# Performance work log

Measured on AMD Instinct MI355X. Metric: run time of the kernel, lower is better.

## Reference

```python
import jax, jax.numpy as jnp
import numpy as np

B, N, D, E, L = 8, 4096, 256, 65536, 1  # graphs, padded nodes, d_model, padded edges, num_layers


def setup_inputs() -> dict:
    key = jax.random.key(0)
    ks = jax.random.split(key, 9)
    x = jax.random.normal(ks[0], (B, N, D), dtype=jnp.float32)
    edge_index = jax.random.randint(ks[1], (B, 2, E), 0, N)
    edge_weight = jax.random.uniform(ks[2], (B, E), dtype=jnp.float32)
    mask = jax.random.randint(ks[3], (B, N), 0, 2).astype(jnp.int32)
    s = 1.0 / np.sqrt(D)
    # GatedGraphConv per-layer linear weight [L, D, D]
    W = jax.random.uniform(ks[4], (L, D, D), jnp.float32, -s, s)
    # GRUCell parameters (r, z, n stacked)
    W_ih = jax.random.uniform(ks[5], (3 * D, D), jnp.float32, -s, s)
    W_hh = jax.random.uniform(ks[6], (3 * D, D), jnp.float32, -s, s)
    b_ih = jax.random.uniform(ks[7], (3 * D,), jnp.float32, -s, s)
    b_hh = jax.random.uniform(ks[8], (3 * D,), jnp.float32, -s, s)
    return {"x": x, "edge_index": edge_index, "edge_weight": edge_weight,
            "mask": mask, "W": W, "W_ih": W_ih, "W_hh": W_hh,
            "b_ih": b_ih, "b_hh": b_hh}


def _gated_graph_conv(x, u, v, ew, W, W_ih, W_hh, b_ih, b_hh):
    """x:[B,N,D]; u,v:[B,E] src/dst indices; ew:[B,E] (already masked)."""
    h = x
    for l in range(L):
        m = jnp.einsum('bnd,de->bne', h, W[l])            # linear transform
        msg = jnp.take_along_axis(m, u[..., None], axis=1) * ew[..., None]  # [B,E,D]
        agg = jax.vmap(lambda ms, vi: jax.ops.segment_sum(ms, vi, num_segments=N))(msg, v)
        # GRUCell(input=agg, hidden=h)
        gi = agg @ W_ih.T + b_ih                          # [B,N,3D]
        gh = h @ W_hh.T + b_hh
        r = jax.nn.sigmoid(gi[..., :D] + gh[..., :D])
        z = jax.nn.sigmoid(gi[..., D:2 * D] + gh[..., D:2 * D])
        n = jnp.tanh(gi[..., 2 * D:] + r * gh[..., 2 * D:])
        h = (1.0 - z) * n + z * h
    return h


def reference(x, edge_index, edge_weight, mask, W, W_ih, W_hh, b_ih, b_hh):
    node_valid = mask > 0                                  # [B,N]
    u = edge_index[:, 0]                                   # source
    v = edge_index[:, 1]                                   # target
    # Drop edges touching invalid nodes: weight -> 0 (equivalent under sum aggr)
    e_valid = jnp.take_along_axis(node_valid, u, axis=1) & jnp.take_along_axis(node_valid, v, axis=1)
    ew = edge_weight * e_valid.astype(edge_weight.dtype)
    h = _gated_graph_conv(x, u, v, ew, W, W_ih, W_hh, b_ih, b_hh)
    # Invalid nodes stay zero (original writes only valid rows of a zeros output)
    return h * node_valid[..., None].astype(h.dtype)
```

## Files before the change

### kernel.cpp

```cpp
#include <hip/hip_runtime.h>
#include <math.h>

#define Bn 8
#define Nn 4096
#define Dn 256
#define En 65536
#define CAP 48

typedef __bf16 bf8 __attribute__((ext_vector_type(8)));
typedef float f4 __attribute__((ext_vector_type(4)));
typedef unsigned short us8 __attribute__((ext_vector_type(8)));

__device__ __forceinline__ float4 ld4(const float* p) { return *(const float4*)p; }

__device__ __forceinline__ unsigned short f2bf(float f) {
    union { float f; unsigned int u; } v; v.f = f;
    unsigned int r = v.u + 0x7fff + ((v.u >> 16) & 1);
    return (unsigned short)(r >> 16);
}
__device__ __forceinline__ float bf2f(unsigned short h) {
    union { unsigned int u; float f; } v; v.u = (unsigned int)h << 16;
    return v.f;
}


__device__ __forceinline__ void stage16c(const unsigned short* __restrict__ gchunk,
                                         int stride, char* ldschunk, int lane) {
    int u = lane >> 3, s = lane & 7;
    int xx = s ^ (u & 7);
    const unsigned short* g = gchunk + (size_t)(2 * u + (xx >> 2)) * stride + (xx & 3) * 8;
    __builtin_amdgcn_global_load_lds((const __attribute__((address_space(1))) void*)g,
                                     (__attribute__((address_space(3))) void*)ldschunk,
                                     16, 0, 0);
}

__device__ __forceinline__ bf8 fragld(const unsigned short* region, int r, int q) {
    int s = (((r & 1) << 2) | q) ^ ((r >> 1) & 7);
    return *(const bf8*)(region + (r >> 1) * 64 + s * 8);
}

__device__ __forceinline__ void ldswrite8(unsigned short* region, int r, int q,
                                          const unsigned short* vals) {
    int s = (((r & 1) << 2) | q) ^ ((r >> 1) & 7);
    *(us8*)(region + (r >> 1) * 64 + s * 8) = *(const us8*)vals;
}


__device__ void rowscan_piece(const int* __restrict__ mask, int* __restrict__ rowidx,
                              int* __restrict__ rowcnt, int* part) {
    int t = threadIdx.x;
    int base = t * 128;
    unsigned long long b0 = 0, b1 = 0;
    int s = 0;
#pragma unroll 8
    for (int i = 0; i < 64; i++) {
        int m = mask[base + i] > 0;
        b0 |= (unsigned long long)m << i; s += m;
    }
#pragma unroll 8
    for (int i = 0; i < 64; i++) {
        int m = mask[base + 64 + i] > 0;
        b1 |= (unsigned long long)m << i; s += m;
    }
    part[t] = s;
    __syncthreads();
    for (int st = 1; st < 256; st <<= 1) {
        int v = (t >= st) ? part[t - st] : 0;
        __syncthreads();
        part[t] += v;
        __syncthreads();
    }
    int run = part[t] - s;
    for (int i = 0; i < 64; i++)
        if ((b0 >> i) & 1) rowidx[run++] = base + i;
    for (int i = 0; i < 64; i++)
        if ((b1 >> i) & 1) rowidx[run++] = base + 64 + i;
    if (t == 255) rowcnt[0] = part[255];
}

__device__ void wf_piece(int wfi, const float* __restrict__ Wih, const float* __restrict__ W,
                         unsigned short* __restrict__ Ball, unsigned short* lds) {
    int t = threadIdx.x, lane = t & 63, w = t >> 6;
    int wr = w >> 1, wc = w & 1, q = lane >> 4, c16 = lane & 15;
    int o0 = (wfi % 6) * 128, d0b = (wfi / 6) * 64;
    f4 acc[4][2];
    f4 zz = {0.f, 0.f, 0.f, 0.f};
#pragma unroll
    for (int rt = 0; rt < 4; rt++)
#pragma unroll
        for (int ct = 0; ct < 2; ct++) acc[rt][ct] = zz;

    int r = t >> 1, half = t & 1;
    for (int k0 = 0; k0 < 256; k0 += 32) {
        const float* pa = Wih + (size_t)(o0 + r) * 256 + k0 + half * 16;
        float4 a0 = ld4(pa), a1 = ld4(pa + 4), a2 = ld4(pa + 8), a3 = ld4(pa + 12);
        float4 b0, b1, b2, b3;
        if (t < 128) {
            const float* pb = W + (size_t)(d0b + r) * 256 + k0 + half * 16;
            b0 = ld4(pb); b1 = ld4(pb + 4); b2 = ld4(pb + 8); b3 = ld4(pb + 12);
        }
        __syncthreads();
        unsigned short tmp[16];
        tmp[0] = f2bf(a0.x); tmp[1] = f2bf(a0.y); tmp[2] = f2bf(a0.z); tmp[3] = f2bf(a0.w);
        tmp[4] = f2bf(a1.x); tmp[5] = f2bf(a1.y); tmp[6] = f2bf(a1.z); tmp[7] = f2bf(a1.w);
        tmp[8] = f2bf(a2.x); tmp[9] = f2bf(a2.y); tmp[10] = f2bf(a2.z); tmp[11] = f2bf(a2.w);
        tmp[12] = f2bf(a3.x); tmp[13] = f2bf(a3.y); tmp[14] = f2bf(a3.z); tmp[15] = f2bf(a3.w);
        ldswrite8(lds, r, half * 2, tmp);
        ldswrite8(lds, r, half * 2 + 1, tmp + 8);
        if (t < 128) {
            unsigned short tb[16];
            tb[0] = f2bf(b0.x); tb[1] = f2bf(b0.y); tb[2] = f2bf(b0.z); tb[3] = f2bf(b0.w);
            tb[4] = f2bf(b1.x); tb[5] = f2bf(b1.y); tb[6] = f2bf(b1.z); tb[7] = f2bf(b1.w);
            tb[8] = f2bf(b2.x); tb[9] = f2bf(b2.y); tb[10] = f2bf(b2.z); tb[11] = f2bf(b2.w);
            tb[12] = f2bf(b3.x); tb[13] = f2bf(b3.y); tb[14] = f2bf(b3.z); tb[15] = f2bf(b3.w);
            ldswrite8(lds + 4096, r, half * 2, tb);
            ldswrite8(lds + 4096, r, half * 2 + 1, tb + 8);
        }
        __syncthreads();
        bf8 a[4];
#pragma unroll
        for (int rt = 0; rt < 4; rt++) a[rt] = fragld(lds, wr * 64 + rt * 16 + c16, q);
#pragma unroll
        for (int ct = 0; ct < 2; ct++) {
            bf8 b = fragld(lds + 4096, wc * 32 + ct * 16 + c16, q);
#pragma unroll
            for (int rt = 0; rt < 4; rt++)
                acc[rt][ct] = __builtin_amdgcn_mfma_f32_16x16x32_bf16(a[rt], b, acc[rt][ct], 0, 0, 0);
        }
    }
#pragma unroll
    for (int ct = 0; ct < 2; ct++) {
        int col = d0b + wc * 32 + ct * 16 + c16;
#pragma unroll
        for (int rt = 0; rt < 4; rt++) {
            int ob = o0 + wr * 64 + rt * 16 + q * 4;
#pragma unroll
            for (int i = 0; i < 4; i++)
                Ball[(size_t)(ob + i) * 512 + col] = f2bf(acc[rt][ct][i]);
        }
    }
}

__global__ __launch_bounds__(256) void setup_kernel(const int* __restrict__ ei,
                                                    const int* __restrict__ mask,
                                                    const float* __restrict__ Wih,
                                                    const float* __restrict__ W,
                                                    const float* __restrict__ Whh,
                                                    const float* __restrict__ ew,
                                                    int* __restrict__ cnt,
                                                    int2* __restrict__ bucket,
                                                    int* __restrict__ rowidx,
                                                    int* __restrict__ rowcnt,
                                                    unsigned short* __restrict__ Ball,
                                                    float* __restrict__ out) {
    __shared__ __align__(16) unsigned short lds[6144];
    int b = blockIdx.x, t = threadIdx.x;
    if (b == 0) {
        rowscan_piece(mask, rowidx, rowcnt, (int*)lds);
        return;
    }
    if (b < 25) {
        wf_piece(b - 1, Wih, W, Ball, lds);
        return;
    }
    if (b < 217) {
        int i = ((b - 25) * 256 + t) * 4;
        float4 wv = ld4(Whh + i);
        int o = i >> 8, d = i & 255;
        ushort4 ov;
        ov.x = f2bf(wv.x); ov.y = f2bf(wv.y); ov.z = f2bf(wv.z); ov.w = f2bf(wv.w);
        *(ushort4*)(Ball + (size_t)o * 512 + 256 + d) = ov;
        return;
    }
    if (b < 2265) {
        int idx = (b - 217) * 256 + t;
        int bb = idx >> 16, e = idx & 65535;
        const int* eb = ei + (size_t)bb * 2 * En;
        int u = eb[e];
        int v = eb[En + e];
        const int* mb = mask + bb * Nn;
        if (mb[u] > 0 && mb[v] > 0) {
            int pos = atomicAdd(&cnt[bb * Nn + v], 1);
            if (pos < CAP) {
                int2 pr;
                pr.x = u;
                pr.y = __float_as_int(ew[(size_t)bb * En + e]);
                bucket[(size_t)(bb * Nn + v) * CAP + pos] = pr;
            }
        }
        return;
    }
    {
        int zb = b - 2265;
        int r = zb * 8 + (t >> 5);
        if (mask[r] > 0) return;
        int col = (t & 31) * 8;
        float4 z = make_float4(0.f, 0.f, 0.f, 0.f);
        *(float4*)(out + (size_t)r * 256 + col) = z;
        *(float4*)(out + (size_t)r * 256 + col + 4) = z;
    }
}


__global__ __launch_bounds__(256) void agg_kernel(const float* __restrict__ x,
                                                  const int* __restrict__ cnt,
                                                  const int2* __restrict__ bucket,
                                                  const int* __restrict__ rowidx,
                                                  const int* __restrict__ rowcnt,
                                                  unsigned short* __restrict__ Ac) {
    int wave = threadIdx.x >> 6, lane = threadIdx.x & 63;
    int i = blockIdx.x * 4 + wave;
    if (i >= rowcnt[0]) return;
    int v = rowidx[i];
    int b = v >> 12, n = v & 4095;
    int m = cnt[b * Nn + n];
    m = m < CAP ? m : CAP;
    const int2* bk = bucket + (size_t)(b * Nn + n) * CAP;
    const float* Xb = x + (size_t)b * Nn * 256;
    float a0 = 0.f, a1 = 0.f, a2 = 0.f, a3 = 0.f;
    for (int j = 0; j < m; j += 8) {
        int u[8]; float wv[8];
#pragma unroll
        for (int k = 0; k < 8; k++) {
            int jj = j + k;
            bool ok = jj < m;
            int2 pr = bk[ok ? jj : 0];
            u[k] = pr.x;
            wv[k] = ok ? __int_as_float(pr.y) : 0.f;
        }
        float4 mv[8];
#pragma unroll
        for (int k = 0; k < 8; k++) mv[k] = ld4(Xb + (size_t)u[k] * 256 + lane * 4);
#pragma unroll
        for (int k = 0; k < 8; k++) {
            a0 += wv[k] * mv[k].x; a1 += wv[k] * mv[k].y;
            a2 += wv[k] * mv[k].z; a3 += wv[k] * mv[k].w;
        }
    }
    ushort4 o;
    o.x = f2bf(a0); o.y = f2bf(a1); o.z = f2bf(a2); o.w = f2bf(a3);
    *(ushort4*)(Ac + (size_t)i * 512 + lane * 4) = o;
    float4 xv = ld4(x + (size_t)v * 256 + lane * 4);
    ushort4 xo;
    xo.x = f2bf(xv.x); xo.y = f2bf(xv.y); xo.z = f2bf(xv.z); xo.w = f2bf(xv.w);
    *(ushort4*)(Ac + (size_t)i * 512 + 256 + lane * 4) = xo;
}


#define GRU_STAGE(kk, bufbase)                                                      \
    {                                                                               \
        if (w < 4) {                                                                \
            _Pragma("unroll") for (int j = 0; j < 3; j++) {                         \
                int c = w * 3 + j;                                                  \
                const unsigned short* src;                                          \
                if (c < 8)                                                          \
                    src = Ac + (size_t)(row0 + c * 16) * 512 + (kk) * 32;           \
                else {                                                              \
                    int g = (c - 8) >> 2, cg = (c - 8) & 3;                         \
                    src = Ball + (size_t)(g * 256 + d0 + cg * 16) * 512 + (kk) * 32;\
                }                                                                   \
                stage16c(src, 512, (char*)(bufbase) + c * 1024, lane);              \
            }                                                                       \
        } else {                                                                    \
            _Pragma("unroll") for (int j = 0; j < 2; j++) {                         \
                int c = 12 + (w - 4) * 2 + j;                                       \
                int g = (c - 8) >> 2, cg = (c - 8) & 3;                             \
                const unsigned short* src =                                         \
                    Ball + (size_t)(g * 256 + d0 + cg * 16) * 512 + (kk) * 32;      \
                stage16c(src, 512, (char*)(bufbase) + c * 1024, lane);              \
            }                                                                       \
        }                                                                           \
    }

#define GRU_COMPUTE(bufbase, ACCM)                                                  \
    {                                                                               \
        const unsigned short* rb = (bufbase);                                       \
        bf8 a0 = fragld(rb + (wr * 2) * 512, c16, q);                               \
        bf8 a1 = fragld(rb + (wr * 2 + 1) * 512, c16, q);                           \
        _Pragma("unroll") for (int ct = 0; ct < 2; ct++) {                          \
            int cg = wc * 2 + ct;                                                   \
            bf8 br = fragld(rb + (8 + cg) * 512, c16, q);                           \
            bf8 bz = fragld(rb + (12 + cg) * 512, c16, q);                          \
            bf8 bm = fragld(rb + (16 + cg) * 512, c16, q);                          \
            acc_r[0][ct] = __builtin_amdgcn_mfma_f32_16x16x32_bf16(a0, br, acc_r[0][ct], 0, 0, 0); \
            acc_r[1][ct] = __builtin_amdgcn_mfma_f32_16x16x32_bf16(a1, br, acc_r[1][ct], 0, 0, 0); \
            acc_z[0][ct] = __builtin_amdgcn_mfma_f32_16x16x32_bf16(a0, bz, acc_z[0][ct], 0, 0, 0); \
            acc_z[1][ct] = __builtin_amdgcn_mfma_f32_16x16x32_bf16(a1, bz, acc_z[1][ct], 0, 0, 0); \
            ACCM[0][ct] = __builtin_amdgcn_mfma_f32_16x16x32_bf16(a0, bm, ACCM[0][ct], 0, 0, 0);   \
            ACCM[1][ct] = __builtin_amdgcn_mfma_f32_16x16x32_bf16(a1, bm, ACCM[1][ct], 0, 0, 0);   \
        }                                                                           \
    }

#define GRU_WAITV(n04, n47)                                                         \
    if (w < 4) { asm volatile("s_waitcnt vmcnt(" #n04 ")" ::: "memory"); }          \
    else       { asm volatile("s_waitcnt vmcnt(" #n47 ")" ::: "memory"); }          \
    __builtin_amdgcn_sched_barrier(0);

#define GRU_STEP(kk, STAGEBUF, COMPBUF, ACCM, n04, n47)                             \
    __builtin_amdgcn_s_barrier();             \
    GRU_STAGE((kk) + 2, STAGEBUF)                                                   \
    GRU_WAITV(n04, n47)                             \
    __builtin_amdgcn_s_barrier();                   \
    __builtin_amdgcn_s_setprio(1);                                                  \
    GRU_COMPUTE(COMPBUF, ACCM)                                                      \
    __builtin_amdgcn_s_setprio(0);                                                  \
    __builtin_amdgcn_sched_barrier(0);

#define GRU_STEP_LAST(kk, COMPBUF, ACCM, n04, n47)                                  \
    __builtin_amdgcn_s_barrier();                                                   \
    GRU_WAITV(n04, n47)                                                             \
    __builtin_amdgcn_s_barrier();                                                   \
    __builtin_amdgcn_s_setprio(1);                                                  \
    GRU_COMPUTE(COMPBUF, ACCM)                                                      \
    __builtin_amdgcn_s_setprio(0);                                                  \
    __builtin_amdgcn_sched_barrier(0);

__global__ __launch_bounds__(512, 4) void gru_kernel(const unsigned short* __restrict__ Ac,
                                                     const unsigned short* __restrict__ Ball,
                                                     const float* __restrict__ bih,
                                                     const float* __restrict__ bhh,
                                                     const int* __restrict__ rowidx,
                                                     const int* __restrict__ rowcnt,
                                                     float* __restrict__ out) {
    __shared__ __align__(16) unsigned short lds[30720];
    const int t = threadIdx.x;
    const int lane = t & 63, w = t >> 6;
    const int wr = w >> 1, wc = w & 1;
    const int q = lane >> 4, c16 = lane & 15;
    const int row0 = blockIdx.x * 128, d0 = blockIdx.y * 64;
    const int cnt = rowcnt[0];
    if (row0 >= cnt) return;

    f4 acc_r[2][2], acc_z[2][2], acc_gn[2][2], acc_hn[2][2];
    f4 zz = {0.f, 0.f, 0.f, 0.f};
#pragma unroll
    for (int rt = 0; rt < 2; rt++)
#pragma unroll
        for (int ct = 0; ct < 2; ct++) {
            acc_r[rt][ct] = zz; acc_z[rt][ct] = zz;
            acc_gn[rt][ct] = zz; acc_hn[rt][ct] = zz;
        }

    unsigned short* bufA = lds;
    unsigned short* bufB = lds + 10240;
    unsigned short* bufC = lds + 20480;

    GRU_STAGE(0, bufA)
    GRU_STAGE(1, bufB)

    GRU_STEP(0,  bufC, bufA, acc_gn, 6, 4)
    GRU_STEP(1,  bufA, bufB, acc_gn, 6, 4)
    GRU_STEP(2,  bufB, bufC, acc_gn, 6, 4)
    GRU_STEP(3,  bufC, bufA, acc_gn, 6, 4)
    GRU_STEP(4,  bufA, bufB, acc_gn, 6, 4)
    GRU_STEP(5,  bufB, bufC, acc_gn, 6, 4)
    GRU_STEP(6,  bufC, bufA, acc_gn, 6, 4)
    GRU_STEP(7,  bufA, bufB, acc_gn, 6, 4)
    GRU_STEP(8,  bufB, bufC, acc_hn, 6, 4)
    GRU_STEP(9,  bufC, bufA, acc_hn, 6, 4)
    GRU_STEP(10, bufA, bufB, acc_hn, 6, 4)
    GRU_STEP(11, bufB, bufC, acc_hn, 6, 4)
    GRU_STEP(12, bufC, bufA, acc_hn, 6, 4)
    GRU_STEP(13, bufA, bufB, acc_hn, 6, 4)
    GRU_STEP_LAST(14, bufC, acc_hn, 3, 2)
    GRU_STEP_LAST(15, bufA, acc_hn, 0, 0)

#pragma unroll
    for (int ct = 0; ct < 2; ct++) {
        int dd = d0 + wc * 32 + ct * 16 + c16;
        float b_r = bih[dd] + bhh[dd];
        float b_z = bih[dd + 256] + bhh[dd + 256];
        float b_gn = bih[dd + 512];
        float b_hn = bhh[dd + 512];
#pragma unroll
        for (int rt = 0; rt < 2; rt++) {
            int rbase = row0 + wr * 32 + rt * 16 + q * 4;
#pragma unroll
            for (int i = 0; i < 4; i++) {
                int rc = rbase + i;
                if (rc < cnt) {
                    float sr = acc_r[rt][ct][i] + b_r;
                    float sz = acc_z[rt][ct][i] + b_z;
                    float gn = acc_gn[rt][ct][i] + b_gn;
                    float hn = acc_hn[rt][ct][i] + b_hn;
                    float rg = 1.f / (1.f + __expf(-sr));
                    float zg = 1.f / (1.f + __expf(-sz));
                    float pre = gn + rg * hn;
                    float e2 = __expf(2.f * pre);
                    float ng = 1.f - 2.f / (e2 + 1.f);
                    float xv = bf2f(Ac[(size_t)rc * 512 + 256 + dd]);
                    float h = (1.f - zg) * ng + zg * xv;
                    int v = rowidx[rc];
                    out[(size_t)v * 256 + dd] = h;
                }
            }
        }
    }
}


extern "C" void kernel_launch(void* const* d_in, const int* in_sizes, int n_in,
                              void* d_out, int out_size, void* d_ws, size_t ws_size,
                              hipStream_t stream) {
    const float* x   = (const float*)d_in[0];
    const int*   ei  = (const int*)d_in[1];
    const float* ew  = (const float*)d_in[2];
    const int*   msk = (const int*)d_in[3];
    const float* W   = (const float*)d_in[4];
    const float* Wih = (const float*)d_in[5];
    const float* Whh = (const float*)d_in[6];
    const float* bih = (const float*)d_in[7];
    const float* bhh = (const float*)d_in[8];
    float* out = (float*)d_out;

    char* p = (char*)d_ws;
    unsigned short* Ac   = (unsigned short*)p; p += (size_t)Bn * Nn * 512 * 2;
    unsigned short* Ball = (unsigned short*)p; p += (size_t)768 * 512 * 2;
    int2* bucket = (int2*)p;  p += (size_t)Bn * Nn * CAP * sizeof(int2);
    int* cnt    = (int*)p;    p += (size_t)Bn * Nn * sizeof(int);
    int* rowidx = (int*)p;    p += (size_t)Bn * Nn * sizeof(int);
    int* rowcnt = (int*)p;    p += 128;

    hipMemsetAsync(cnt, 0, (size_t)Bn * Nn * sizeof(int), stream);
    setup_kernel<<<6361, 256, 0, stream>>>(ei, msk, Wih, W, Whh, ew, cnt, bucket,
                                           rowidx, rowcnt, Ball, out);
    agg_kernel<<<(Bn * Nn) / 4, 256, 0, stream>>>(x, cnt, bucket, rowidx, rowcnt, Ac);
    gru_kernel<<<dim3(256, 4), 512, 0, stream>>>(Ac, Ball, bih, bhh, rowidx, rowcnt, out);
}
```

Before: 166.1 us.

## Pin agg blocks per graph to XCDs and narrow GRU tile for occupancy

The aggregation kernel now assigns blocks by graph index (blockIdx & 7), so each XCD handles one graph's rows and its slice of x stays local to that XCD's L2. Per-graph row offsets come from new partial counts written by the setup kernel. The GRU kernel halves the output column tile to 32, which doubles the grid in y, shrinks LDS use and accumulators, and raises the occupancy bound to 6. It also remaps row blocks so consecutive tiles land on the same XCD. In exchange, the smaller tile re-reads the A operand twice as often and the staging work is split differently across waves.

```diff
diff --git a/kernel.cpp b/kernel.cpp
--- a/kernel.cpp
+++ b/kernel.cpp
@@ -75,6 +75,7 @@
         if ((b0 >> i) & 1) rowidx[run++] = base + i;
     for (int i = 0; i < 64; i++)
         if ((b1 >> i) & 1) rowidx[run++] = base + 64 + i;
+    if ((t & 31) == 31) rowcnt[1 + (t >> 5)] = part[t];
     if (t == 255) rowcnt[0] = part[255];
 }
 
@@ -209,66 +210,70 @@
                                                   const int* __restrict__ rowcnt,
                                                   unsigned short* __restrict__ Ac) {
     int wave = threadIdx.x >> 6, lane = threadIdx.x & 63;
-    int i = blockIdx.x * 4 + wave;
-    if (i >= rowcnt[0]) return;
-    int v = rowidx[i];
-    int b = v >> 12, n = v & 4095;
-    int m = cnt[b * Nn + n];
-    m = m < CAP ? m : CAP;
-    const int2* bk = bucket + (size_t)(b * Nn + n) * CAP;
+    int b = blockIdx.x & 7;
+    int slot = blockIdx.x >> 3;
+    int p0 = (b == 0) ? 0 : rowcnt[b];
+    int p1 = rowcnt[b + 1];
+    const int2* bkb = bucket + (size_t)b * Nn * CAP;
+    const int* cntb = cnt + b * Nn;
     const float* Xb = x + (size_t)b * Nn * 256;
-    float a0 = 0.f, a1 = 0.f, a2 = 0.f, a3 = 0.f;
-    for (int j = 0; j < m; j += 8) {
-        int u[8]; float wv[8];
-#pragma unroll
-        for (int k = 0; k < 8; k++) {
-            int jj = j + k;
-            bool ok = jj < m;
-            int2 pr = bk[ok ? jj : 0];
-            u[k] = pr.x;
-            wv[k] = ok ? __int_as_float(pr.y) : 0.f;
-        }
-        float4 mv[8];
-#pragma unroll
-        for (int k = 0; k < 8; k++) mv[k] = ld4(Xb + (size_t)u[k] * 256 + lane * 4);
-#pragma unroll
-        for (int k = 0; k < 8; k++) {
-            a0 += wv[k] * mv[k].x; a1 += wv[k] * mv[k].y;
-            a2 += wv[k] * mv[k].z; a3 += wv[k] * mv[k].w;
-        }
-    }
-    ushort4 o;
-    o.x = f2bf(a0); o.y = f2bf(a1); o.z = f2bf(a2); o.w = f2bf(a3);
-    *(ushort4*)(Ac + (size_t)i * 512 + lane * 4) = o;
-    float4 xv = ld4(x + (size_t)v * 256 + lane * 4);
-    ushort4 xo;
-    xo.x = f2bf(xv.x); xo.y = f2bf(xv.y); xo.z = f2bf(xv.z); xo.w = f2bf(xv.w);
-    *(ushort4*)(Ac + (size_t)i * 512 + 256 + lane * 4) = xo;
+    for (int i = p0 + slot * 4 + wave; i < p1; i += 4 * 512) {
+        int v = rowidx[i];
+        int n = v & 4095;
+        float4 xv = ld4(Xb + (size_t)n * 256 + lane * 4);
+        int m = cntb[n];
+        m = m < CAP ? m : CAP;
+        const int2* bk = bkb + (size_t)n * CAP;
+        float a0 = 0.f, a1 = 0.f, a2 = 0.f, a3 = 0.f;
+        for (int j = 0; j < m; j += 8) {
+            int u[8]; float wv[8];
+#pragma unroll
+            for (int k = 0; k < 8; k++) {
+                int jj = j + k;
+                bool ok = jj < m;
+                int2 pr = bk[ok ? jj : 0];
+                u[k] = pr.x;
+                wv[k] = ok ? __int_as_float(pr.y) : 0.f;
+            }
+            float4 mv[8];
+#pragma unroll
+            for (int k = 0; k < 8; k++) mv[k] = ld4(Xb + (size_t)u[k] * 256 + lane * 4);
+#pragma unroll
+            for (int k = 0; k < 8; k++) {
+                a0 += wv[k] * mv[k].x; a1 += wv[k] * mv[k].y;
+                a2 += wv[k] * mv[k].z; a3 += wv[k] * mv[k].w;
+            }
+        }
+        ushort4 o;
+        o.x = f2bf(a0); o.y = f2bf(a1); o.z = f2bf(a2); o.w = f2bf(a3);
+        *(ushort4*)(Ac + (size_t)i * 512 + lane * 4) = o;
+        ushort4 xo;
+        xo.x = f2bf(xv.x); xo.y = f2bf(xv.y); xo.z = f2bf(xv.z); xo.w = f2bf(xv.w);
+        *(ushort4*)(Ac + (size_t)i * 512 + 256 + lane * 4) = xo;
+    }
 }
 
 
 #define GRU_STAGE(kk, bufbase)                                                      \
     {                                                                               \
-        if (w < 4) {                                                                \
-            _Pragma("unroll") for (int j = 0; j < 3; j++) {                         \
-                int c = w * 3 + j;                                                  \
+        if (w < 6) {                                                                \
+            _Pragma("unroll") for (int j = 0; j < 2; j++) {                         \
+                int c = w * 2 + j;                                                  \
                 const unsigned short* src;                                          \
                 if (c < 8)                                                          \
                     src = Ac + (size_t)(row0 + c * 16) * 512 + (kk) * 32;           \
                 else {                                                              \
-                    int g = (c - 8) >> 2, cg = (c - 8) & 3;                         \
-                    src = Ball + (size_t)(g * 256 + d0 + cg * 16) * 512 + (kk) * 32;\
+                    int idx = c - 8, g = idx >> 1, h = idx & 1;                     \
+                    src = Ball + (size_t)(g * 256 + d0 + h * 16) * 512 + (kk) * 32; \
                 }                                                                   \
                 stage16c(src, 512, (char*)(bufbase) + c * 1024, lane);              \
             }                                                                       \
         } else {                                                                    \
-            _Pragma("unroll") for (int j = 0; j < 2; j++) {                         \
-                int c = 12 + (w - 4) * 2 + j;                                       \
-                int g = (c - 8) >> 2, cg = (c - 8) & 3;                             \
-                const unsigned short* src =                                         \
-                    Ball + (size_t)(g * 256 + d0 + cg * 16) * 512 + (kk) * 32;      \
-                stage16c(src, 512, (char*)(bufbase) + c * 1024, lane);              \
-            }                                                                       \
+            int c = 12 + (w - 6);                                                   \
+            int idx = c - 8, g = idx >> 1, h = idx & 1;                             \
+            const unsigned short* src =                                             \
+                Ball + (size_t)(g * 256 + d0 + h * 16) * 512 + (kk) * 32;           \
+            stage16c(src, 512, (char*)(bufbase) + c * 1024, lane);                  \
         }                                                                           \
     }
 
@@ -277,97 +282,95 @@
         const unsigned short* rb = (bufbase);                                       \
         bf8 a0 = fragld(rb + (wr * 2) * 512, c16, q);                               \
         bf8 a1 = fragld(rb + (wr * 2 + 1) * 512, c16, q);                           \
-        _Pragma("unroll") for (int ct = 0; ct < 2; ct++) {                          \
-            int cg = wc * 2 + ct;                                                   \
-            bf8 br = fragld(rb + (8 + cg) * 512, c16, q);                           \
-            bf8 bz = fragld(rb + (12 + cg) * 512, c16, q);                          \
-            bf8 bm = fragld(rb + (16 + cg) * 512, c16, q);                          \
-            acc_r[0][ct] = __builtin_amdgcn_mfma_f32_16x16x32_bf16(a0, br, acc_r[0][ct], 0, 0, 0); \
-            acc_r[1][ct] = __builtin_amdgcn_mfma_f32_16x16x32_bf16(a1, br, acc_r[1][ct], 0, 0, 0); \
-            acc_z[0][ct] = __builtin_amdgcn_mfma_f32_16x16x32_bf16(a0, bz, acc_z[0][ct], 0, 0, 0); \
-            acc_z[1][ct] = __builtin_amdgcn_mfma_f32_16x16x32_bf16(a1, bz, acc_z[1][ct], 0, 0, 0); \
-            ACCM[0][ct] = __builtin_amdgcn_mfma_f32_16x16x32_bf16(a0, bm, ACCM[0][ct], 0, 0, 0);   \
-            ACCM[1][ct] = __builtin_amdgcn_mfma_f32_16x16x32_bf16(a1, bm, ACCM[1][ct], 0, 0, 0);   \
-        }                                                                           \
-    }
-
-#define GRU_WAITV(n04, n47)                                                         \
-    if (w < 4) { asm volatile("s_waitcnt vmcnt(" #n04 ")" ::: "memory"); }          \
-    else       { asm volatile("s_waitcnt vmcnt(" #n47 ")" ::: "memory"); }          \
+        bf8 br = fragld(rb + (8 + wc) * 512, c16, q);                               \
+        bf8 bz = fragld(rb + (10 + wc) * 512, c16, q);                              \
+        bf8 bm = fragld(rb + (12 + wc) * 512, c16, q);                              \
+        acc_r[0] = __builtin_amdgcn_mfma_f32_16x16x32_bf16(a0, br, acc_r[0], 0, 0, 0); \
+        acc_r[1] = __builtin_amdgcn_mfma_f32_16x16x32_bf16(a1, br, acc_r[1], 0, 0, 0); \
+        acc_z[0] = __builtin_amdgcn_mfma_f32_16x16x32_bf16(a0, bz, acc_z[0], 0, 0, 0); \
+        acc_z[1] = __builtin_amdgcn_mfma_f32_16x16x32_bf16(a1, bz, acc_z[1], 0, 0, 0); \
+        ACCM[0] = __builtin_amdgcn_mfma_f32_16x16x32_bf16(a0, bm, ACCM[0], 0, 0, 0);   \
+        ACCM[1] = __builtin_amdgcn_mfma_f32_16x16x32_bf16(a1, bm, ACCM[1], 0, 0, 0);   \
+    }
+
+#define GRU_WAITV(n05, n67)                                                         \
+    if (w < 6) { asm volatile("s_waitcnt vmcnt(" #n05 ")" ::: "memory"); }          \
+    else       { asm volatile("s_waitcnt vmcnt(" #n67 ")" ::: "memory"); }          \
     __builtin_amdgcn_sched_barrier(0);
 
-#define GRU_STEP(kk, STAGEBUF, COMPBUF, ACCM, n04, n47)                             \
+#define GRU_STEP(kk, STAGEBUF, COMPBUF, ACCM)                                       \
     __builtin_amdgcn_s_barrier();             \
     GRU_STAGE((kk) + 2, STAGEBUF)                                                   \
-    GRU_WAITV(n04, n47)                             \
+    GRU_WAITV(4, 2)                                 \
     __builtin_amdgcn_s_barrier();                   \
     __builtin_amdgcn_s_setprio(1);                                                  \
     GRU_COMPUTE(COMPBUF, ACCM)                                                      \
     __builtin_amdgcn_s_setprio(0);                                                  \
     __builtin_amdgcn_sched_barrier(0);
 
-#define GRU_STEP_LAST(kk, COMPBUF, ACCM, n04, n47)                                  \
+#define GRU_STEP_LAST(kk, COMPBUF, ACCM, n05, n67)                                  \
     __builtin_amdgcn_s_barrier();                                                   \
-    GRU_WAITV(n04, n47)                                                             \
+    GRU_WAITV(n05, n67)                                                             \
     __builtin_amdgcn_s_barrier();                                                   \
     __builtin_amdgcn_s_setprio(1);                                                  \
     GRU_COMPUTE(COMPBUF, ACCM)                                                      \
     __builtin_amdgcn_s_setprio(0);                                                  \
     __builtin_amdgcn_sched_barrier(0);
 
-__global__ __launch_bounds__(512, 4) void gru_kernel(const unsigned short* __restrict__ Ac,
+__global__ __launch_bounds__(512, 6) void gru_kernel(const unsigned short* __restrict__ Ac,
                                                      const unsigned short* __restrict__ Ball,
                                                      const float* __restrict__ bih,
                                                      const float* __restrict__ bhh,
                                                      const int* __restrict__ rowidx,
                                                      const int* __restrict__ rowcnt,
                                                      float* __restrict__ out) {
-    __shared__ __align__(16) unsigned short lds[30720];
+    __shared__ __align__(16) unsigned short lds[21504];
     const int t = threadIdx.x;
     const int lane = t & 63, w = t >> 6;
     const int wr = w >> 1, wc = w & 1;
     const int q = lane >> 4, c16 = lane & 15;
-    const int row0 = blockIdx.x * 128, d0 = blockIdx.y * 64;
     const int cnt = rowcnt[0];
-    if (row0 >= cnt) return;
-
-    f4 acc_r[2][2], acc_z[2][2], acc_gn[2][2], acc_hn[2][2];
+    const int nact = (cnt + 127) >> 7;
+    if (blockIdx.x >= nact) return;
+    int q8 = nact >> 3, r8 = nact & 7;
+    int xcd = blockIdx.x & 7, jj = blockIdx.x >> 3;
+    int xp = (xcd < r8 ? xcd * (q8 + 1) : r8 * (q8 + 1) + (xcd - r8) * q8) + jj;
+    const int row0 = xp * 128, d0 = blockIdx.y * 32;
+
+    f4 acc_r[2], acc_z[2], acc_gn[2], acc_hn[2];
     f4 zz = {0.f, 0.f, 0.f, 0.f};
 #pragma unroll
-    for (int rt = 0; rt < 2; rt++)
-#pragma unroll
-        for (int ct = 0; ct < 2; ct++) {
-            acc_r[rt][ct] = zz; acc_z[rt][ct] = zz;
-            acc_gn[rt][ct] = zz; acc_hn[rt][ct] = zz;
-        }
+    for (int rt = 0; rt < 2; rt++) {
+        acc_r[rt] = zz; acc_z[rt] = zz;
+        acc_gn[rt] = zz; acc_hn[rt] = zz;
+    }
 
     unsigned short* bufA = lds;
-    unsigned short* bufB = lds + 10240;
-    unsigned short* bufC = lds + 20480;
+    unsigned short* bufB = lds + 7168;
+    unsigned short* bufC = lds + 14336;
 
     GRU_STAGE(0, bufA)
     GRU_STAGE(1, bufB)
 
-    GRU_STEP(0,  bufC, bufA, acc_gn, 6, 4)
-    GRU_STEP(1,  bufA, bufB, acc_gn, 6, 4)
-    GRU_STEP(2,  bufB, bufC, acc_gn, 6, 4)
-    GRU_STEP(3,  bufC, bufA, acc_gn, 6, 4)
-    GRU_STEP(4,  bufA, bufB, acc_gn, 6, 4)
-    GRU_STEP(5,  bufB, bufC, acc_gn, 6, 4)
-    GRU_STEP(6,  bufC, bufA, acc_gn, 6, 4)
-    GRU_STEP(7,  bufA, bufB, acc_gn, 6, 4)
-    GRU_STEP(8,  bufB, bufC, acc_hn, 6, 4)
-    GRU_STEP(9,  bufC, bufA, acc_hn, 6, 4)
-    GRU_STEP(10, bufA, bufB, acc_hn, 6, 4)
-    GRU_STEP(11, bufB, bufC, acc_hn, 6, 4)
-    GRU_STEP(12, bufC, bufA, acc_hn, 6, 4)
-    GRU_STEP(13, bufA, bufB, acc_hn, 6, 4)
-    GRU_STEP_LAST(14, bufC, acc_hn, 3, 2)
+    GRU_STEP(0,  bufC, bufA, acc_gn)
+    GRU_STEP(1,  bufA, bufB, acc_gn)
+    GRU_STEP(2,  bufB, bufC, acc_gn)
+    GRU_STEP(3,  bufC, bufA, acc_gn)
+    GRU_STEP(4,  bufA, bufB, acc_gn)
+    GRU_STEP(5,  bufB, bufC, acc_gn)
+    GRU_STEP(6,  bufC, bufA, acc_gn)
+    GRU_STEP(7,  bufA, bufB, acc_gn)
+    GRU_STEP(8,  bufB, bufC, acc_hn)
+    GRU_STEP(9,  bufC, bufA, acc_hn)
+    GRU_STEP(10, bufA, bufB, acc_hn)
+    GRU_STEP(11, bufB, bufC, acc_hn)
+    GRU_STEP(12, bufC, bufA, acc_hn)
+    GRU_STEP(13, bufA, bufB, acc_hn)
+    GRU_STEP_LAST(14, bufC, acc_hn, 2, 1)
     GRU_STEP_LAST(15, bufA, acc_hn, 0, 0)
 
-#pragma unroll
-    for (int ct = 0; ct < 2; ct++) {
-        int dd = d0 + wc * 32 + ct * 16 + c16;
+    {
+        int dd = d0 + wc * 16 + c16;
         float b_r = bih[dd] + bhh[dd];
         float b_z = bih[dd + 256] + bhh[dd + 256];
         float b_gn = bih[dd + 512];
@@ -379,10 +382,10 @@
             for (int i = 0; i < 4; i++) {
                 int rc = rbase + i;
                 if (rc < cnt) {
-                    float sr = acc_r[rt][ct][i] + b_r;
-                    float sz = acc_z[rt][ct][i] + b_z;
-                    float gn = acc_gn[rt][ct][i] + b_gn;
-                    float hn = acc_hn[rt][ct][i] + b_hn;
+                    float sr = acc_r[rt][i] + b_r;
+                    float sz = acc_z[rt][i] + b_z;
+                    float gn = acc_gn[rt][i] + b_gn;
+                    float hn = acc_hn[rt][i] + b_hn;
                     float rg = 1.f / (1.f + __expf(-sr));
                     float zg = 1.f / (1.f + __expf(-sz));
                     float pre = gn + rg * hn;
@@ -424,6 +427,6 @@
     hipMemsetAsync(cnt, 0, (size_t)Bn * Nn * sizeof(int), stream);
     setup_kernel<<<6361, 256, 0, stream>>>(ei, msk, Wih, W, Whh, ew, cnt, bucket,
                                            rowidx, rowcnt, Ball, out);
-    agg_kernel<<<(Bn * Nn) / 4, 256, 0, stream>>>(x, cnt, bucket, rowidx, rowcnt, Ac);
-    gru_kernel<<<dim3(256, 4), 512, 0, stream>>>(Ac, Ball, bih, bhh, rowidx, rowcnt, out);
-}
+    agg_kernel<<<8 * 512, 256, 0, stream>>>(x, cnt, bucket, rowidx, rowcnt, Ac);
+    gru_kernel<<<dim3(256, 8), 512, 0, stream>>>(Ac, Ball, bih, bhh, rowidx, rowcnt, out);
+}
```

New measurement: 160.7 us. -3.3%, faster.
